# Kernel tuning notes

Hardware: AMD Instinct MI355X
Metric: run time of the kernel (lower is better)

The kernel has to match this reference:

```python
import jax, jax.numpy as jnp
import numpy as np

EPS_NORM = 1e-8   # torch cosine_similarity norm eps
EPS_DEN = 1e-10
CLAMP_MAX = 1e10


def _cos_matrix(a, b):
    # rows of a vs rows of b: [Na, Nb] cosine similarity via normalized matmul
    an = a / jnp.clip(jnp.linalg.norm(a, axis=-1, keepdims=True), EPS_NORM)
    bn = b / jnp.clip(jnp.linalg.norm(b, axis=-1, keepdims=True), EPS_NORM)
    return an @ bn.T


def setup_inputs() -> dict:
    key = jax.random.key(0)
    k1, k2, k3, k4, k5 = jax.random.split(key, 5)
    N, D, M, C = 4096, 256, 2, 100
    return {
        "label_encodings": jax.random.normal(k1, (N, D), dtype=jnp.float32),
        "fusion_z": jax.random.normal(k2, (M, N, D), dtype=jnp.float32),
        "sample_embeddings": jax.random.normal(k3, (N, D), dtype=jnp.float32),
        "label_embeddings": jax.random.normal(k4, (N, D), dtype=jnp.float32),
        "labels": jax.random.randint(k5, (N,), 0, C, dtype=jnp.int64),
        "temperature": jnp.ones((), dtype=jnp.float32),
        "xi": jnp.ones((), dtype=jnp.float32),
    }


def reference(label_encodings, fusion_z, sample_embeddings, label_embeddings,
              labels, temperature, xi):
    # ---- class_prompt_contrastive_Learning ----
    sim = _cos_matrix(label_encodings, label_encodings)            # [N, N]
    e = jnp.minimum(jnp.exp(sim / temperature), CLAMP_MAX)
    mask = (labels[:, None] == labels[None, :])
    num = jnp.sum(e * mask, axis=1)
    den = jnp.clip(jnp.sum(e, axis=1), EPS_DEN)
    loss_class = jnp.mean(-jnp.log(num / den))

    # ---- supervised_cross_view_contrastive ----
    M, N, D = fusion_z.shape
    fz = fusion_z.reshape(M * N, D)
    lab_exp = jnp.tile(labels, M)                                  # labels.repeat(M)
    mask2 = (lab_exp[:, None] == lab_exp[None, :])
    sim2 = _cos_matrix(fz, fz)                                     # [MN, MN]
    e2 = jnp.exp(sim2 / temperature)
    num2 = jnp.sum(e2 * mask2, axis=1)
    den2 = jnp.clip(jnp.sum(e2, axis=1), EPS_DEN)
    loss_cross = jnp.mean(-jnp.log(num2 / den2))

    # ---- boundary_aware_independent_hashing ----
    cs = _cos_matrix(sample_embeddings, label_embeddings)          # [N, N]
    Dm = (1.0 - cs) * 0.5
    y = (labels[:, None] == labels[None, :]).astype(cs.dtype)
    loss_mat = y * Dm ** 2 + (1.0 - y) * jnp.maximum(xi - Dm, 0.0) ** 2
    loss_hash = jnp.mean(loss_mat)

    return jnp.stack([loss_class, loss_cross, loss_hash])
```

## Files before the change

### kernel.cpp

```cpp
#include <hip/hip_runtime.h>
#include <hip/hip_bf16.h>
#include <stdint.h>


typedef __attribute__((ext_vector_type(8))) short bf16x8;
typedef __attribute__((ext_vector_type(4))) float f32x4;

__device__ inline void gload_lds16(const void* g, void* l) {
  __builtin_amdgcn_global_load_lds(
      (__attribute__((address_space(1))) void*)g,
      (__attribute__((address_space(3))) void*)l, 16, 0, 0);
}

__device__ inline void barrier_raw() {
  asm volatile("" ::: "memory");
  __builtin_amdgcn_s_barrier();
  asm volatile("" ::: "memory");
}

__device__ inline unsigned short f2bf(float x) {
  unsigned int u = __builtin_bit_cast(unsigned int, x);
  u = (u + 0x7fffu + ((u >> 16) & 1u)) >> 16;
  return (unsigned short)u;
}

__global__ __launch_bounds__(256) void norm_kernel(
    const float* __restrict__ LE, const float* __restrict__ FZ,
    const float* __restrict__ SE, const float* __restrict__ LM,
    unsigned short* __restrict__ An, unsigned short* __restrict__ Fn,
    unsigned short* __restrict__ Sn, unsigned short* __restrict__ Ln,
    float* __restrict__ hacc, float* __restrict__ out) {
  const int tid = threadIdx.x;
  if (blockIdx.x == 0) {
    if (tid == 0) out[0] = 0.f;
    if (tid == 1) out[1] = 0.f;
    if (tid == 2) hacc[0] = 0.f;
  }

  const int wid = tid >> 6, lane = tid & 63;
  const int row = blockIdx.x * 4 + wid;

  const float* src;
  unsigned short* dst;
  int r;
  if (row < 4096)       { src = LE; dst = An; r = row; }
  else if (row < 12288) { src = FZ; dst = Fn; r = row - 4096; }
  else if (row < 16384) { src = SE; dst = Sn; r = row - 12288; }
  else                  { src = LM; dst = Ln; r = row - 16384; }

  const float4 v = *(const float4*)(src + (size_t)r * 256 + lane * 4);
  float ss = v.x * v.x + v.y * v.y + v.z * v.z + v.w * v.w;
#pragma unroll
  for (int m = 1; m < 64; m <<= 1) ss += __shfl_xor(ss, m);
  const float scale = 1.0f / fmaxf(sqrtf(ss), 1e-8f);

  ushort4 o;
  o.x = f2bf(v.x * scale);
  o.y = f2bf(v.y * scale);
  o.z = f2bf(v.z * scale);
  o.w = f2bf(v.w * scale);
  *(ushort4*)(dst + (size_t)r * 256 + lane * 4) = o;
}

__device__ inline void tri_decode(int t, int nb, int& rb, int& cb) {
  int r = 0;
  while (t >= nb - r) { t -= nb - r; ++r; }
  rb = r;
  cb = r + t;
}

__global__ __launch_bounds__(512, 4) void fused_sim(
    const unsigned short* __restrict__ An, const unsigned short* __restrict__ Fn,
    const unsigned short* __restrict__ Sn, const unsigned short* __restrict__ Ln,
    const int* __restrict__ labels,
    const float* __restrict__ tp, const float* __restrict__ xip,
    float2* __restrict__ Pc,
    float2* __restrict__ Px,
    float* __restrict__ hacc) {
  __shared__ __align__(16) char Ab[2][16384];
  __shared__ __align__(16) char Bb[2][16384];
  __shared__ int lrS[128], lcS[128];

  const int hw = blockIdx.x;
  const int bid = (hw & 7) * 454 + (hw >> 3);

  int mode, rb, cb;
  const unsigned short *X, *Y;
  if (bid < 528) {
    mode = 0; tri_decode(bid, 32, rb, cb); X = An; Y = An;
  } else if (bid < 2608) {
    mode = 1; tri_decode(bid - 528, 64, rb, cb); X = Fn; Y = Fn;
  } else {
    mode = 2; const int t = bid - 2608; rb = t >> 5; cb = t & 31;
    X = Sn; Y = Ln;
  }

  const int tid = threadIdx.x;
  const int lane = tid & 63, wid = tid >> 6;
  const int wr = wid >> 1, wc = wid & 1;
  const int g = lane >> 4, c = lane & 15;

  int mylab = labels[(tid < 128 ? rb * 128 + tid : cb * 128 + tid - 128) & 4095];

  f32x4 acc[2][4];
  const f32x4 zero = {0.f, 0.f, 0.f, 0.f};
#pragma unroll
  for (int m = 0; m < 2; ++m)
#pragma unroll
    for (int n = 0; n < 4; ++n) acc[m][n] = zero;

  const int srow = tid >> 3;
  const int sgl = (tid & 7) ^ (srow & 7);
  const char* xs = (const char*)X + ((size_t)rb * 128 + srow) * 512 + sgl * 16;
  const char* ys = (const char*)Y + ((size_t)cb * 128 + srow) * 512 + sgl * 16;

#define STAGE(KK, BUF)                                                    \
  do {                                                                    \
    const char* xa = xs + (KK) * 128;                                     \
    const char* ya = ys + (KK) * 128;                                     \
    char* da = (char*)(&Ab[(BUF)][0]) + wid * 1024;                       \
    char* db = (char*)(&Bb[(BUF)][0]) + wid * 1024;                       \
    gload_lds16(xa, da);                                                  \
    gload_lds16(xa + 32768, da + 8192);                                   \
    gload_lds16(ya, db);                                                  \
    gload_lds16(ya + 32768, db + 8192);                                   \
  } while (0)

  STAGE(0, 0);
  STAGE(1, 1);
  asm volatile("" : "+v"(mylab));

  const int pxs = c & 7;
  const int aoff = (wr * 32 + c) * 128;
  const int boff = (wc * 64 + c) * 128;

#pragma unroll
  for (int kk = 0; kk < 4; ++kk) {
    if (kk < 3) asm volatile("s_waitcnt vmcnt(4)" ::: "memory");
    else        asm volatile("s_waitcnt vmcnt(0)" ::: "memory");
    barrier_raw();
    if (kk == 0) {
      if (tid < 128)      lrS[tid] = mylab;
      else if (tid < 256) lcS[tid - 128] = mylab;
    }
    const char* ab = (const char*)(&Ab[kk & 1][0]) + aoff;
    const char* bb = (const char*)(&Bb[kk & 1][0]) + boff;
#pragma unroll
    for (int ks = 0; ks < 2; ++ks) {
      const int px = ((ks * 4 + g) ^ pxs) * 16;
      bf16x8 af[2], bg[4];
#pragma unroll
      for (int m = 0; m < 2; ++m) af[m] = *(const bf16x8*)(ab + m * 2048 + px);
#pragma unroll
      for (int n = 0; n < 4; ++n) bg[n] = *(const bf16x8*)(bb + n * 2048 + px);
      __builtin_amdgcn_s_setprio(1);
#pragma unroll
      for (int m = 0; m < 2; ++m)
#pragma unroll
        for (int n = 0; n < 4; ++n)
          acc[m][n] = __builtin_amdgcn_mfma_f32_16x16x32_bf16(
              af[m], bg[n], acc[m][n], 0, 0, 0);
      __builtin_amdgcn_s_setprio(0);
    }
    barrier_raw();
    if (kk < 2) STAGE(kk + 2, kk & 1);
  }
#undef STAGE

  float* sc = (float*)(&Ab[0][0]);
  if (mode < 2) {
    const float invt = 1.0f / tp[0];
    const bool docol = (rb != cb);
    float2* Pp = (mode == 0) ? Pc : Px;
    const int NR = (mode == 0) ? 4096 : 8192;
    int collab[4];
#pragma unroll
    for (int n = 0; n < 4; ++n) collab[n] = lcS[wc * 64 + n * 16 + c];

    float* rowN = sc, *rowD = sc + 256, *colN = sc + 512, *colD = sc + 1024;
    float cn[4] = {0.f, 0.f, 0.f, 0.f}, cd[4] = {0.f, 0.f, 0.f, 0.f};
    float rn[8], rd[8];
#pragma unroll
    for (int m = 0; m < 2; ++m) {
#pragma unroll
      for (int reg = 0; reg < 4; ++reg) {
        const int rlab = lrS[wr * 32 + m * 16 + g * 4 + reg];
        float pn = 0.f, pd = 0.f;
#pragma unroll
        for (int n = 0; n < 4; ++n) {
          float e = __expf(acc[m][n][reg] * invt);
          if (mode == 0) e = fminf(e, 1e10f);
          pd += e;
          const float en = (rlab == collab[n]) ? e : 0.f;
          pn += en;
          cd[n] += e;
          cn[n] += en;
        }
#pragma unroll
        for (int msk = 1; msk < 16; msk <<= 1) {
          pn += __shfl_xor(pn, msk);
          pd += __shfl_xor(pd, msk);
        }
        rn[m * 4 + reg] = pn;
        rd[m * 4 + reg] = pd;
      }
    }
    if (c == 0) {
#pragma unroll
      for (int m = 0; m < 2; ++m)
#pragma unroll
        for (int reg = 0; reg < 4; ++reg) {
          const int rloc = wr * 32 + m * 16 + g * 4 + reg;
          rowN[wc * 128 + rloc] = rn[m * 4 + reg];
          rowD[wc * 128 + rloc] = rd[m * 4 + reg];
        }
    }
#pragma unroll
    for (int n = 0; n < 4; ++n) {
      float a = cn[n], b = cd[n];
      a += __shfl_xor(a, 16); b += __shfl_xor(b, 16);
      a += __shfl_xor(a, 32); b += __shfl_xor(b, 32);
      if (g == 0) {
        colN[wr * 128 + wc * 64 + n * 16 + c] = a;
        colD[wr * 128 + wc * 64 + n * 16 + c] = b;
      }
    }
    __syncthreads();
    if (tid < 128) {
      Pp[(size_t)cb * NR + rb * 128 + tid] =
          make_float2(rowN[tid] + rowN[128 + tid], rowD[tid] + rowD[128 + tid]);
    } else if (tid < 256 && docol) {
      const int t2 = tid - 128;
      Pp[(size_t)rb * NR + cb * 128 + t2] = make_float2(
          colN[t2] + colN[128 + t2] + colN[256 + t2] + colN[384 + t2],
          colD[t2] + colD[128 + t2] + colD[256 + t2] + colD[384 + t2]);
    }
  } else {
    const float xi = xip[0];
    int collab[4];
#pragma unroll
    for (int n = 0; n < 4; ++n) collab[n] = lcS[wc * 64 + n * 16 + c];
    float part = 0.f;
#pragma unroll
    for (int m = 0; m < 2; ++m)
#pragma unroll
      for (int reg = 0; reg < 4; ++reg) {
        const int rlab = lrS[wr * 32 + m * 16 + g * 4 + reg];
#pragma unroll
        for (int n = 0; n < 4; ++n) {
          const float cs = acc[m][n][reg];
          const float Dm = (1.0f - cs) * 0.5f;
          const float u = fmaxf(xi - Dm, 0.0f);
          part += (rlab == collab[n]) ? Dm * Dm : u * u;
        }
      }
#pragma unroll
    for (int msk = 1; msk < 64; msk <<= 1) part += __shfl_xor(part, msk);
    if (lane == 0) sc[wid] = part;
    __syncthreads();
    if (tid == 0) {
      float s = 0.f;
#pragma unroll
      for (int w = 0; w < 8; ++w) s += sc[w];
      atomicAdd(hacc, s);
    }
  }
}

__global__ __launch_bounds__(256) void finalize_kernel(
    const float2* __restrict__ Pc, const float2* __restrict__ Px,
    const float* __restrict__ hacc, float* __restrict__ out) {
  const int b = blockIdx.x, tid = threadIdx.x;
  const float2* P;
  int nslots, NR, row, oi;
  if (b < 16) { P = Pc; nslots = 32; NR = 4096; row = b * 256 + tid; oi = 0; }
  else { P = Px; nslots = 64; NR = 8192; row = (b - 16) * 256 + tid; oi = 1; }
  float n = 0.f, d = 0.f;
  for (int s = 0; s < nslots; ++s) {
    const float2 v = P[(size_t)s * NR + row];
    n += v.x;
    d += v.y;
  }
  float val = -logf(n / fmaxf(d, 1e-10f));
#pragma unroll
  for (int m = 1; m < 64; m <<= 1) val += __shfl_xor(val, m);
  __shared__ float r[4];
  if ((tid & 63) == 0) r[tid >> 6] = val;
  __syncthreads();
  if (tid == 0) atomicAdd(&out[oi], (r[0] + r[1] + r[2] + r[3]) / (float)NR);
  if (b == 0 && tid == 0) out[2] = hacc[0] * (1.0f / 16777216.0f);
}

extern "C" void kernel_launch(void* const* d_in, const int* in_sizes, int n_in,
                              void* d_out, int out_size, void* d_ws,
                              size_t ws_size, hipStream_t stream) {
  const float* LE = (const float*)d_in[0];
  const float* FZ = (const float*)d_in[1];
  const float* SE = (const float*)d_in[2];
  const float* LM = (const float*)d_in[3];
  const int* labels = (const int*)d_in[4];
  const float* tp = (const float*)d_in[5];
  const float* xip = (const float*)d_in[6];
  float* out = (float*)d_out;

  char* ws = (char*)d_ws;
  unsigned short* An = (unsigned short*)(ws);
  unsigned short* Fn = (unsigned short*)(ws + 2097152);
  unsigned short* Sn = (unsigned short*)(ws + 6291456);
  unsigned short* Ln = (unsigned short*)(ws + 8388608);
  float2* Pc = (float2*)(ws + 10485760);
  float2* Px = (float2*)(ws + 11534336);
  float* hacc = (float*)(ws + 15728640);

  norm_kernel<<<dim3(5120), dim3(256), 0, stream>>>(LE, FZ, SE, LM, An, Fn,
                                                    Sn, Ln, hacc, out);
  fused_sim<<<dim3(3632), dim3(512), 0, stream>>>(An, Fn, Sn, Ln, labels, tp,
                                                  xip, Pc, Px, hacc);
  finalize_kernel<<<dim3(48), dim3(256), 0, stream>>>(Pc, Px, hacc, out);
}
```

Baseline: 172.4 us.

## Make fused_sim persistent and prefetch next tile during epilogue

Result: no change. 172.7 us (+0.1%).

```diff
diff --git a/kernel.cpp b/kernel.cpp
--- a/kernel.cpp
+++ b/kernel.cpp
@@ -14,6 +14,12 @@
 
 __device__ inline void barrier_raw() {
   asm volatile("" ::: "memory");
+  __builtin_amdgcn_s_barrier();
+  asm volatile("" ::: "memory");
+}
+
+__device__ inline void lgkm_barrier() {
+  asm volatile("s_waitcnt lgkmcnt(0)" ::: "memory");
   __builtin_amdgcn_s_barrier();
   asm volatile("" ::: "memory");
 }
@@ -69,6 +75,20 @@
   cb = r + t;
 }
 
+__device__ inline void decode_tile(
+    int bid, const unsigned short* An, const unsigned short* Fn,
+    const unsigned short* Sn, const unsigned short* Ln, int& mode, int& rb,
+    int& cb, const unsigned short*& X, const unsigned short*& Y) {
+  if (bid < 528) {
+    mode = 0; tri_decode(bid, 32, rb, cb); X = An; Y = An;
+  } else if (bid < 2608) {
+    mode = 1; tri_decode(bid - 528, 64, rb, cb); X = Fn; Y = Fn;
+  } else {
+    mode = 2; const int t = bid - 2608; rb = t >> 5; cb = t & 31;
+    X = Sn; Y = Ln;
+  }
+}
+
 __global__ __launch_bounds__(512, 4) void fused_sim(
     const unsigned short* __restrict__ An, const unsigned short* __restrict__ Fn,
     const unsigned short* __restrict__ Sn, const unsigned short* __restrict__ Ln,
@@ -80,44 +100,35 @@
   __shared__ __align__(16) char Ab[2][16384];
   __shared__ __align__(16) char Bb[2][16384];
   __shared__ int lrS[128], lcS[128];
-
-  const int hw = blockIdx.x;
-  const int bid = (hw & 7) * 454 + (hw >> 3);
-
-  int mode, rb, cb;
-  const unsigned short *X, *Y;
-  if (bid < 528) {
-    mode = 0; tri_decode(bid, 32, rb, cb); X = An; Y = An;
-  } else if (bid < 2608) {
-    mode = 1; tri_decode(bid - 528, 64, rb, cb); X = Fn; Y = Fn;
-  } else {
-    mode = 2; const int t = bid - 2608; rb = t >> 5; cb = t & 31;
-    X = Sn; Y = Ln;
-  }
+  __shared__ float sN[256], sD[256], cN[512], cD[512];
 
   const int tid = threadIdx.x;
   const int lane = tid & 63, wid = tid >> 6;
   const int wr = wid >> 1, wc = wid & 1;
   const int g = lane >> 4, c = lane & 15;
 
-  int mylab = labels[(tid < 128 ? rb * 128 + tid : cb * 128 + tid - 128) & 4095];
-
-  f32x4 acc[2][4];
-  const f32x4 zero = {0.f, 0.f, 0.f, 0.f};
-#pragma unroll
-  for (int m = 0; m < 2; ++m)
-#pragma unroll
-    for (int n = 0; n < 4; ++n) acc[m][n] = zero;
+  const int hw = blockIdx.x;
+  int bid = (hw & 7) * 64 + (hw >> 3);
 
   const int srow = tid >> 3;
   const int sgl = (tid & 7) ^ (srow & 7);
+  const int pxs = c & 7;
+  const int aoff = (wr * 32 + c) * 128;
+  const int boff = (wc * 64 + c) * 128;
+
+  const float invt = 1.0f / tp[0];
+  const float xi = xip[0];
+
+  int mode, rb, cb;
+  const unsigned short *X, *Y;
+  decode_tile(bid, An, Fn, Sn, Ln, mode, rb, cb, X, Y);
   const char* xs = (const char*)X + ((size_t)rb * 128 + srow) * 512 + sgl * 16;
   const char* ys = (const char*)Y + ((size_t)cb * 128 + srow) * 512 + sgl * 16;
 
-#define STAGE(KK, BUF)                                                    \
+#define STAGE(PX, PY, KK, BUF)                                            \
   do {                                                                    \
-    const char* xa = xs + (KK) * 128;                                     \
-    const char* ya = ys + (KK) * 128;                                     \
+    const char* xa = (PX) + (KK) * 128;                                   \
+    const char* ya = (PY) + (KK) * 128;                                   \
     char* da = (char*)(&Ab[(BUF)][0]) + wid * 1024;                       \
     char* db = (char*)(&Bb[(BUF)][0]) + wid * 1024;                       \
     gload_lds16(xa, da);                                                  \
@@ -126,145 +137,177 @@
     gload_lds16(ya + 32768, db + 8192);                                   \
   } while (0)
 
-  STAGE(0, 0);
-  STAGE(1, 1);
+  int mylab =
+      labels[(tid < 128 ? rb * 128 + tid : cb * 128 + tid - 128) & 4095];
+  STAGE(xs, ys, 0, 0);
+  STAGE(xs, ys, 1, 1);
   asm volatile("" : "+v"(mylab));
 
-  const int pxs = c & 7;
-  const int aoff = (wr * 32 + c) * 128;
-  const int boff = (wc * 64 + c) * 128;
-
-#pragma unroll
-  for (int kk = 0; kk < 4; ++kk) {
-    if (kk < 3) asm volatile("s_waitcnt vmcnt(4)" ::: "memory");
-    else        asm volatile("s_waitcnt vmcnt(0)" ::: "memory");
-    barrier_raw();
-    if (kk == 0) {
-      if (tid < 128)      lrS[tid] = mylab;
-      else if (tid < 256) lcS[tid - 128] = mylab;
+  f32x4 acc[2][4];
+  const f32x4 zero = {0.f, 0.f, 0.f, 0.f};
+
+  while (true) {
+    const int nbid = bid + 512;
+    const bool has_next = (nbid < 3632);
+    int nmode = 0, nrb = 0, ncb = 0;
+    const unsigned short *nX = nullptr, *nY = nullptr;
+    const char *nxs = nullptr, *nys = nullptr;
+    if (has_next) {
+      decode_tile(nbid, An, Fn, Sn, Ln, nmode, nrb, ncb, nX, nY);
+      nxs = (const char*)nX + ((size_t)nrb * 128 + srow) * 512 + sgl * 16;
+      nys = (const char*)nY + ((size_t)ncb * 128 + srow) * 512 + sgl * 16;
     }
-    const char* ab = (const char*)(&Ab[kk & 1][0]) + aoff;
-    const char* bb = (const char*)(&Bb[kk & 1][0]) + boff;
-#pragma unroll
-    for (int ks = 0; ks < 2; ++ks) {
-      const int px = ((ks * 4 + g) ^ pxs) * 16;
-      bf16x8 af[2], bg[4];
-#pragma unroll
-      for (int m = 0; m < 2; ++m) af[m] = *(const bf16x8*)(ab + m * 2048 + px);
-#pragma unroll
-      for (int n = 0; n < 4; ++n) bg[n] = *(const bf16x8*)(bb + n * 2048 + px);
-      __builtin_amdgcn_s_setprio(1);
+
+#pragma unroll
+    for (int m = 0; m < 2; ++m)
+#pragma unroll
+      for (int n = 0; n < 4; ++n) acc[m][n] = zero;
+
+#pragma unroll
+    for (int kk = 0; kk < 4; ++kk) {
+      if (kk == 3 && !has_next) {
+        asm volatile("s_waitcnt vmcnt(0)" ::: "memory");
+      } else {
+        asm volatile("s_waitcnt vmcnt(4)" ::: "memory");
+      }
+      barrier_raw();
+      if (kk == 0) {
+        if (tid < 128)      lrS[tid] = mylab;
+        else if (tid < 256) lcS[tid - 128] = mylab;
+      }
+      const char* ab = (const char*)(&Ab[kk & 1][0]) + aoff;
+      const char* bb = (const char*)(&Bb[kk & 1][0]) + boff;
+#pragma unroll
+      for (int ks = 0; ks < 2; ++ks) {
+        const int px = ((ks * 4 + g) ^ pxs) * 16;
+        bf16x8 af[2], bg[4];
+#pragma unroll
+        for (int m = 0; m < 2; ++m)
+          af[m] = *(const bf16x8*)(ab + m * 2048 + px);
+#pragma unroll
+        for (int n = 0; n < 4; ++n)
+          bg[n] = *(const bf16x8*)(bb + n * 2048 + px);
+        __builtin_amdgcn_s_setprio(1);
+#pragma unroll
+        for (int m = 0; m < 2; ++m)
+#pragma unroll
+          for (int n = 0; n < 4; ++n)
+            acc[m][n] = __builtin_amdgcn_mfma_f32_16x16x32_bf16(
+                af[m], bg[n], acc[m][n], 0, 0, 0);
+        __builtin_amdgcn_s_setprio(0);
+      }
+      barrier_raw();
+      if (kk < 2) {
+        STAGE(xs, ys, kk + 2, kk & 1);
+      } else if (kk == 2 && has_next) {
+        mylab = labels[(tid < 128 ? nrb * 128 + tid : ncb * 128 + tid - 128) &
+                       4095];
+        STAGE(nxs, nys, 0, 0);
+        asm volatile("" : "+v"(mylab));
+      }
+    }
+    if (has_next) STAGE(nxs, nys, 1, 1);
+
+    if (mode < 2) {
+      const bool docol = (rb != cb);
+      float2* Pp = (mode == 0) ? Pc : Px;
+      const int NR = (mode == 0) ? 4096 : 8192;
+      int collab[4];
+#pragma unroll
+      for (int n = 0; n < 4; ++n) collab[n] = lcS[wc * 64 + n * 16 + c];
+
+      float cn[4] = {0.f, 0.f, 0.f, 0.f}, cd[4] = {0.f, 0.f, 0.f, 0.f};
+      float rn[8], rd[8];
+#pragma unroll
+      for (int m = 0; m < 2; ++m) {
+#pragma unroll
+        for (int reg = 0; reg < 4; ++reg) {
+          const int rlab = lrS[wr * 32 + m * 16 + g * 4 + reg];
+          float pn = 0.f, pd = 0.f;
+#pragma unroll
+          for (int n = 0; n < 4; ++n) {
+            float e = __expf(acc[m][n][reg] * invt);
+            if (mode == 0) e = fminf(e, 1e10f);
+            pd += e;
+            const float en = (rlab == collab[n]) ? e : 0.f;
+            pn += en;
+            cd[n] += e;
+            cn[n] += en;
+          }
+#pragma unroll
+          for (int msk = 1; msk < 16; msk <<= 1) {
+            pn += __shfl_xor(pn, msk);
+            pd += __shfl_xor(pd, msk);
+          }
+          rn[m * 4 + reg] = pn;
+          rd[m * 4 + reg] = pd;
+        }
+      }
+      if (c == 0) {
+#pragma unroll
+        for (int m = 0; m < 2; ++m)
+#pragma unroll
+          for (int reg = 0; reg < 4; ++reg) {
+            const int rloc = wr * 32 + m * 16 + g * 4 + reg;
+            sN[wc * 128 + rloc] = rn[m * 4 + reg];
+            sD[wc * 128 + rloc] = rd[m * 4 + reg];
+          }
+      }
+#pragma unroll
+      for (int n = 0; n < 4; ++n) {
+        float a = cn[n], b = cd[n];
+        a += __shfl_xor(a, 16); b += __shfl_xor(b, 16);
+        a += __shfl_xor(a, 32); b += __shfl_xor(b, 32);
+        if (g == 0) {
+          cN[wr * 128 + wc * 64 + n * 16 + c] = a;
+          cD[wr * 128 + wc * 64 + n * 16 + c] = b;
+        }
+      }
+      lgkm_barrier();
+      if (tid < 128) {
+        Pp[(size_t)cb * NR + rb * 128 + tid] =
+            make_float2(sN[tid] + sN[128 + tid], sD[tid] + sD[128 + tid]);
+      } else if (tid < 256 && docol) {
+        const int t2 = tid - 128;
+        Pp[(size_t)rb * NR + cb * 128 + t2] = make_float2(
+            cN[t2] + cN[128 + t2] + cN[256 + t2] + cN[384 + t2],
+            cD[t2] + cD[128 + t2] + cD[256 + t2] + cD[384 + t2]);
+      }
+    } else {
+      int collab[4];
+#pragma unroll
+      for (int n = 0; n < 4; ++n) collab[n] = lcS[wc * 64 + n * 16 + c];
+      float part = 0.f;
 #pragma unroll
       for (int m = 0; m < 2; ++m)
 #pragma unroll
-        for (int n = 0; n < 4; ++n)
-          acc[m][n] = __builtin_amdgcn_mfma_f32_16x16x32_bf16(
-              af[m], bg[n], acc[m][n], 0, 0, 0);
-      __builtin_amdgcn_s_setprio(0);
+        for (int reg = 0; reg < 4; ++reg) {
+          const int rlab = lrS[wr * 32 + m * 16 + g * 4 + reg];
+#pragma unroll
+          for (int n = 0; n < 4; ++n) {
+            const float cs = acc[m][n][reg];
+            const float Dm = (1.0f - cs) * 0.5f;
+            const float u = fmaxf(xi - Dm, 0.0f);
+            part += (rlab == collab[n]) ? Dm * Dm : u * u;
+          }
+        }
+#pragma unroll
+      for (int msk = 1; msk < 64; msk <<= 1) part += __shfl_xor(part, msk);
+      if (lane == 0) sN[wid] = part;
+      lgkm_barrier();
+      if (tid == 0) {
+        float s = 0.f;
+#pragma unroll
+        for (int w = 0; w < 8; ++w) s += sN[w];
+        atomicAdd(hacc, s);
+      }
     }
-    barrier_raw();
-    if (kk < 2) STAGE(kk + 2, kk & 1);
+
+    if (!has_next) break;
+    bid = nbid; mode = nmode; rb = nrb; cb = ncb;
+    xs = nxs; ys = nys;
   }
 #undef STAGE
-
-  float* sc = (float*)(&Ab[0][0]);
-  if (mode < 2) {
-    const float invt = 1.0f / tp[0];
-    const bool docol = (rb != cb);
-    float2* Pp = (mode == 0) ? Pc : Px;
-    const int NR = (mode == 0) ? 4096 : 8192;
-    int collab[4];
-#pragma unroll
-    for (int n = 0; n < 4; ++n) collab[n] = lcS[wc * 64 + n * 16 + c];
-
-    float* rowN = sc, *rowD = sc + 256, *colN = sc + 512, *colD = sc + 1024;
-    float cn[4] = {0.f, 0.f, 0.f, 0.f}, cd[4] = {0.f, 0.f, 0.f, 0.f};
-    float rn[8], rd[8];
-#pragma unroll
-    for (int m = 0; m < 2; ++m) {
-#pragma unroll
-      for (int reg = 0; reg < 4; ++reg) {
-        const int rlab = lrS[wr * 32 + m * 16 + g * 4 + reg];
-        float pn = 0.f, pd = 0.f;
-#pragma unroll
-        for (int n = 0; n < 4; ++n) {
-          float e = __expf(acc[m][n][reg] * invt);
-          if (mode == 0) e = fminf(e, 1e10f);
-          pd += e;
-          const float en = (rlab == collab[n]) ? e : 0.f;
-          pn += en;
-          cd[n] += e;
-          cn[n] += en;
-        }
-#pragma unroll
-        for (int msk = 1; msk < 16; msk <<= 1) {
-          pn += __shfl_xor(pn, msk);
-          pd += __shfl_xor(pd, msk);
-        }
-        rn[m * 4 + reg] = pn;
-        rd[m * 4 + reg] = pd;
-      }
-    }
-    if (c == 0) {
-#pragma unroll
-      for (int m = 0; m < 2; ++m)
-#pragma unroll
-        for (int reg = 0; reg < 4; ++reg) {
-          const int rloc = wr * 32 + m * 16 + g * 4 + reg;
-          rowN[wc * 128 + rloc] = rn[m * 4 + reg];
-          rowD[wc * 128 + rloc] = rd[m * 4 + reg];
-        }
-    }
-#pragma unroll
-    for (int n = 0; n < 4; ++n) {
-      float a = cn[n], b = cd[n];
-      a += __shfl_xor(a, 16); b += __shfl_xor(b, 16);
-      a += __shfl_xor(a, 32); b += __shfl_xor(b, 32);
-      if (g == 0) {
-        colN[wr * 128 + wc * 64 + n * 16 + c] = a;
-        colD[wr * 128 + wc * 64 + n * 16 + c] = b;
-      }
-    }
-    __syncthreads();
-    if (tid < 128) {
-      Pp[(size_t)cb * NR + rb * 128 + tid] =
-          make_float2(rowN[tid] + rowN[128 + tid], rowD[tid] + rowD[128 + tid]);
-    } else if (tid < 256 && docol) {
-      const int t2 = tid - 128;
-      Pp[(size_t)rb * NR + cb * 128 + t2] = make_float2(
-          colN[t2] + colN[128 + t2] + colN[256 + t2] + colN[384 + t2],
-          colD[t2] + colD[128 + t2] + colD[256 + t2] + colD[384 + t2]);
-    }
-  } else {
-    const float xi = xip[0];
-    int collab[4];
-#pragma unroll
-    for (int n = 0; n < 4; ++n) collab[n] = lcS[wc * 64 + n * 16 + c];
-    float part = 0.f;
-#pragma unroll
-    for (int m = 0; m < 2; ++m)
-#pragma unroll
-      for (int reg = 0; reg < 4; ++reg) {
-        const int rlab = lrS[wr * 32 + m * 16 + g * 4 + reg];
-#pragma unroll
-        for (int n = 0; n < 4; ++n) {
-          const float cs = acc[m][n][reg];
-          const float Dm = (1.0f - cs) * 0.5f;
-          const float u = fmaxf(xi - Dm, 0.0f);
-          part += (rlab == collab[n]) ? Dm * Dm : u * u;
-        }
-      }
-#pragma unroll
-    for (int msk = 1; msk < 64; msk <<= 1) part += __shfl_xor(part, msk);
-    if (lane == 0) sc[wid] = part;
-    __syncthreads();
-    if (tid == 0) {
-      float s = 0.f;
-#pragma unroll
-      for (int w = 0; w < 8; ++w) s += sc[w];
-      atomicAdd(hacc, s);
-    }
-  }
 }
 
 __global__ __launch_bounds__(256) void finalize_kernel(
@@ -314,7 +357,7 @@
 
   norm_kernel<<<dim3(5120), dim3(256), 0, stream>>>(LE, FZ, SE, LM, An, Fn,
                                                     Sn, Ln, hacc, out);
-  fused_sim<<<dim3(3632), dim3(512), 0, stream>>>(An, Fn, Sn, Ln, labels, tp,
-                                                  xip, Pc, Px, hacc);
+  fused_sim<<<dim3(512), dim3(512), 0, stream>>>(An, Fn, Sn, Ln, labels, tp,
+                                                 xip, Pc, Px, hacc);
   finalize_kernel<<<dim3(48), dim3(256), 0, stream>>>(Pc, Px, hacc, out);
 }
```
